# Kernel optimization log

Measured on AMD Instinct MI355X. Metric: run time of the kernel, lower is better.

## Reference

```python
import jax, jax.numpy as jnp
import numpy as np

DET = 512       # detector bins
N_THETA = 180   # projection angles, theta = 0..179 degrees (1 deg spacing)


def _ramp_filter(size):
    """skimage _get_fourier_filter(size, 'ramp'): spatial ramp -> FFT."""
    n = np.concatenate((np.arange(1, size // 2 + 1, 2),
                        np.arange(size // 2 - 1, 0, -2)))
    f = np.zeros(size)
    f[0] = 0.25
    f[1::2] = -1.0 / (np.pi * n) ** 2
    return jnp.asarray(2.0 * np.real(np.fft.fft(f)), dtype=jnp.float32)


def _iradon(x):
    B, C, det, A = x.shape
    theta = jnp.deg2rad(jnp.arange(A, dtype=jnp.float32))  # 0..179 deg

    # --- ramp filtering along the detector axis ---
    size = max(64, int(2 ** np.ceil(np.log2(2 * det))))  # 1024 for det=512
    filt = _ramp_filter(size)                            # (size,)
    xp = jnp.pad(x, ((0, 0), (0, 0), (0, size - det), (0, 0)))
    proj_f = jnp.fft.fft(xp, axis=2) * filt[None, None, :, None]
    filtered = jnp.real(jnp.fft.ifft(proj_f, axis=2))[:, :, :det, :]  # (B,C,det,A)

    # --- backprojection (circle=False) ---
    out_size = int(np.floor(np.sqrt(det ** 2 / 2.0)))  # 362
    radius = out_size // 2
    xpr = jnp.arange(out_size, dtype=jnp.float32)[:, None] - radius  # rows
    ypr = jnp.arange(out_size, dtype=jnp.float32)[None, :] - radius  # cols
    cos_t = jnp.cos(theta)
    sin_t = jnp.sin(theta)
    # detector coordinate for every (angle, pixel): t = y*cos - x*sin
    t = ypr[None] * cos_t[:, None, None] - xpr[None] * sin_t[:, None, None]  # (A,out,out)
    pos = t + det // 2          # index into detector axis (x = arange(det)-det//2)
    i0 = jnp.floor(pos).astype(jnp.int32)
    frac = pos - i0.astype(jnp.float32)
    in_range = ((pos >= 0) & (pos <= det - 1)).astype(jnp.float32)  # fill_value=0 outside
    i0c = jnp.clip(i0, 0, det - 1)
    i1c = jnp.clip(i0 + 1, 0, det - 1)

    P = out_size * out_size
    ft = jnp.moveaxis(filtered, 3, 2)                     # (B,C,A,det)
    idx0 = jnp.broadcast_to(i0c.reshape(A, P)[None, None], (B, C, A, P))
    idx1 = jnp.broadcast_to(i1c.reshape(A, P)[None, None], (B, C, A, P))
    g0 = jnp.take_along_axis(ft, idx0, axis=3)            # (B,C,A,P)
    g1 = jnp.take_along_axis(ft, idx1, axis=3)
    w = frac.reshape(A, P)[None, None]
    m = in_range.reshape(A, P)[None, None]
    val = ((1.0 - w) * g0 + w * g1) * m                   # bilinear-in-1D interp, 0 outside
    recon = val.sum(axis=2).reshape(B, C, out_size, out_size)
    return recon * (jnp.pi / (2.0 * A))


def setup_inputs() -> dict:
    key = jax.random.key(0)
    x = jax.random.normal(key, (4, 1, DET, N_THETA), dtype=jnp.float32)
    return {"x": x}


def reference(x):
    return _iradon(x)
```

## Files before the change

kernel.cpp:

```cpp
#include <hip/hip_runtime.h>
#include <math.h>

#define DET 512
#define NA  180
#define OUT 362
#define RAD 181
#define OUTSQ (OUT * OUT)
#define NB  4

#define NSPLIT 12
#define APB    15
#define CHUNK  3
#define LSTR   5
#define LLEN   (514 * LSTR)

constexpr double PI_D = 3.14159265358979323846;

constexpr double tsin(double x) {
    double x2 = x * x;
    return x * (1.0 + x2 * (-1.0/6 + x2 * (1.0/120 + x2 * (-1.0/5040 +
               x2 * (1.0/362880 + x2 * (-1.0/39916800))))));
}
constexpr double tcos(double x) {
    double x2 = x * x;
    return 1.0 + x2 * (-0.5 + x2 * (1.0/24 + x2 * (-1.0/720 +
               x2 * (1.0/40320 + x2 * (-1.0/3628800)))));
}

struct Trig { float c[NA]; float s[NA]; };
constexpr Trig make_trig() {
    Trig t{};
    constexpr double r = PI_D / 180.0;
    for (int k = 0; k < NA; ++k) {
        double c, s;
        if (k <= 45)       { c =  tcos(k * r);          s =  tsin(k * r); }
        else if (k <= 90)  { c =  tsin((90 - k) * r);   s =  tcos((90 - k) * r); }
        else if (k <= 135) { c = -tsin((k - 90) * r);   s =  tcos((k - 90) * r); }
        else               { c = -tcos((180 - k) * r);  s =  tsin((180 - k) * r); }
        t.c[k] = (float)c; t.s[k] = (float)s;
    }
    return t;
}
__device__ constexpr Trig TRIG = make_trig();

__host__ __device__ constexpr float rampw0(int m) {
    int a = m < 0 ? -m : m;
    if (a > 511 || (a & 1) == 0) return 0.0f;
    double md = (double)a;
    return (float)(-2.0 / (PI_D * PI_D * md * md));
}

template<int R>
__device__ __forceinline__ void tap(const float* __restrict__ p,
        float& a0, float& a1, float& a2, float& a3) {
    const float v = p[R];
    if constexpr (rampw0(R)      != 0.0f) a0 = fmaf(rampw0(R),      v, a0);
    if constexpr (rampw0(R - 32) != 0.0f) a1 = fmaf(rampw0(R - 32), v, a1);
    if constexpr (rampw0(R - 64) != 0.0f) a2 = fmaf(rampw0(R - 64), v, a2);
    if constexpr (rampw0(R - 96) != 0.0f) a3 = fmaf(rampw0(R - 96), v, a3);
}

template<int R, int REND>
__device__ __forceinline__ void sweep(const float* __restrict__ p,
        float& a0, float& a1, float& a2, float& a3) {
    if constexpr (R <= REND) {
        tap<R>(p, a0, a1, a2, a3);
        sweep<R + 2, REND>(p, a0, a1, a2, a3);
    }
}

__global__ __launch_bounds__(256) void ramp_filter_kernel(
        const float* __restrict__ x, float* __restrict__ ft) {
    const int a   = blockIdx.x;
    const int b   = blockIdx.y;
    const int tid = threadIdx.x;
    const int t    = tid & 127;
    const int half = tid >> 7;
    const int q = (t & 31) + 128 * (t >> 5);

    __shared__ float xs[3 * DET];
    __shared__ float red[4 * 128];

    xs[tid]        = 0.0f;
    xs[256 + tid]  = 0.0f;
    xs[1024 + tid] = 0.0f;
    xs[1280 + tid] = 0.0f;
    xs[512 + tid]  = x[(b * DET + tid) * NA + a];
    xs[768 + tid]  = x[(b * DET + 256 + tid) * NA + a];
    __syncthreads();

    const float* p = xs + 512 + q;
    float a0 = 0.0f, a1 = 0.0f, a2 = 0.0f, a3 = 0.0f;

    if (half == 0) {
        a0 = 0.5f * p[0];
        a1 = 0.5f * p[32];
        a2 = 0.5f * p[64];
        a3 = 0.5f * p[96];
        sweep<-511, 47>(p, a0, a1, a2, a3);
    } else {
        sweep<49, 607>(p, a0, a1, a2, a3);
        red[      t] = a0;
        red[128 + t] = a1;
        red[256 + t] = a2;
        red[384 + t] = a3;
    }
    __syncthreads();

    if (half == 0) {
        float* ob = ft + ((size_t)a * DET + q) * NB + b;
        ob[0]           = a0 + red[      t];
        ob[32 * NB]     = a1 + red[128 + t];
        ob[64 * NB]     = a2 + red[256 + t];
        ob[96 * NB]     = a3 + red[384 + t];
    }
}

__device__ __forceinline__ void acc4(float4& acc,
        const float* __restrict__ L, float pos) {
    float pf = floorf(pos);
    float fr = pos - pf;
    int   i0 = (int)pf;
    int   di = (pos > (float)(DET - 1)) ? (DET * LSTR) : (i0 * LSTR);
    const float* qp = L + di;
    float g0x = qp[0],        g0y = qp[1],        g0z = qp[2],        g0w = qp[3];
    float g1x = qp[LSTR + 0], g1y = qp[LSTR + 1], g1z = qp[LSTR + 2], g1w = qp[LSTR + 3];
    acc.x += fmaf(fr, g1x - g0x, g0x);
    acc.y += fmaf(fr, g1y - g0y, g0y);
    acc.z += fmaf(fr, g1z - g0z, g0z);
    acc.w += fmaf(fr, g1w - g0w, g0w);
}

__global__ __launch_bounds__(256) void backproject_kernel(
        const float4* __restrict__ ftq, float* __restrict__ out) {
    const int sp = blockIdx.z;
    const int r0 = blockIdx.y * 32;
    const int c0 = blockIdx.x * 32;
    const int tid = threadIdx.x;
    const int tx = tid & 15;
    const int ty = tid >> 4;

    __shared__ float lines[CHUNK][LLEN];

    if (tid < CHUNK * 10)
        lines[tid / 10][512 * LSTR + (tid % 10)] = 0.0f;

    const float xpr = (float)(min(r0 + ty, OUT - 1) - RAD);
    const float ypr = (float)(min(c0 + tx, OUT - 1) - RAD);

    float4 A00 = {0,0,0,0}, A01 = {0,0,0,0}, A10 = {0,0,0,0}, A11 = {0,0,0,0};

    for (int rd = 0; rd < APB / CHUNK; ++rd) {
        __syncthreads();
        const float4* g = ftq + (size_t)(sp * APB + rd * CHUNK) * DET;
        #pragma unroll
        for (int k = 0; k < CHUNK * DET / 256; ++k) {
            int j = tid + k * 256;
            float4 v = g[j];
            float* w = &lines[j >> 9][(j & 511) * LSTR];
            w[0] = v.x; w[1] = v.y; w[2] = v.z; w[3] = v.w;
        }
        __syncthreads();

        const int abase = sp * APB + rd * CHUNK;
        #pragma unroll
        for (int i = 0; i < CHUNK; ++i) {
            const float cv = TRIG.c[abase + i];
            const float sv = TRIG.s[abase + i];
            float p00 = fmaf(ypr, cv, fmaf(xpr, -sv, 256.0f));
            float p01 = fmaf(16.0f, cv, p00);
            float p10 = fmaf(-16.0f, sv, p00);
            float p11 = fmaf(-16.0f, sv, p01);
            const float* L = &lines[i][0];
            acc4(A00, L, p00);
            acc4(A01, L, p01);
            acc4(A10, L, p10);
            acc4(A11, L, p11);
        }
    }

    const float scale = (float)(PI_D / (2.0 * NA));
    const int r = r0 + ty;
    const int c = c0 + tx;

#define EMIT(ACC, RR, CC)                                          \
    if ((RR) < OUT && (CC) < OUT) {                                \
        const int off = (RR) * OUT + (CC);                         \
        atomicAdd(out + off,             (ACC).x * scale);         \
        atomicAdd(out + OUTSQ + off,     (ACC).y * scale);         \
        atomicAdd(out + 2 * OUTSQ + off, (ACC).z * scale);         \
        atomicAdd(out + 3 * OUTSQ + off, (ACC).w * scale);         \
    }
    EMIT(A00, r, c);
    EMIT(A01, r, c + 16);
    EMIT(A10, r + 16, c);
    EMIT(A11, r + 16, c + 16);
#undef EMIT
}

extern "C" void kernel_launch(void* const* d_in, const int* in_sizes, int n_in,
                              void* d_out, int out_size, void* d_ws, size_t ws_size,
                              hipStream_t stream) {
    const float* x = (const float*)d_in[0];
    float* ft  = (float*)d_ws;
    float* out = (float*)d_out;

    const int B = in_sizes[0] / (DET * NA);

    hipMemsetAsync(out, 0, (size_t)out_size * sizeof(float), stream);
    ramp_filter_kernel<<<dim3(NA, B), 256, 0, stream>>>(x, ft);
    backproject_kernel<<<dim3((OUT + 31) / 32, (OUT + 31) / 32, NSPLIT),
                         256, 0, stream>>>((const float4*)ft, out);
}
```

Baseline: 111.2 us.

## Gather backprojection samples directly from global memory instead of LDS staging

Removes the shared-memory staging of detector lines and the per-chunk barriers, so each thread now reads float4 samples straight from global memory and relies on the L1/L2 caches. Out-of-range handling becomes an index clamp plus a multiplicative mask instead of a padded zero entry. The angle split also changes from 12 to 15 splits of 12 angles, which adds blocks and atomics. The gathers now pay global or cache latency rather than LDS latency, and fewer angles per block means more atomic traffic.

Result: slower. 125.8 us (+13.2%).

```diff
diff --git a/kernel.cpp b/kernel.cpp
--- a/kernel.cpp
+++ b/kernel.cpp
@@ -8,11 +8,8 @@
 #define OUTSQ (OUT * OUT)
 #define NB  4
 
-#define NSPLIT 12
-#define APB    15
-#define CHUNK  3
-#define LSTR   5
-#define LLEN   (514 * LSTR)
+#define NSPLIT 15
+#define APB    12
 
 constexpr double PI_D = 3.14159265358979323846;
 
@@ -116,19 +113,18 @@
     }
 }
 
-__device__ __forceinline__ void acc4(float4& acc,
-        const float* __restrict__ L, float pos) {
-    float pf = floorf(pos);
-    float fr = pos - pf;
-    int   i0 = (int)pf;
-    int   di = (pos > (float)(DET - 1)) ? (DET * LSTR) : (i0 * LSTR);
-    const float* qp = L + di;
-    float g0x = qp[0],        g0y = qp[1],        g0z = qp[2],        g0w = qp[3];
-    float g1x = qp[LSTR + 0], g1y = qp[LSTR + 1], g1z = qp[LSTR + 2], g1w = qp[LSTR + 3];
-    acc.x += fmaf(fr, g1x - g0x, g0x);
-    acc.y += fmaf(fr, g1y - g0y, g0y);
-    acc.z += fmaf(fr, g1z - g0z, g0z);
-    acc.w += fmaf(fr, g1w - g0w, g0w);
+__device__ __forceinline__ void acc4g(float4& acc,
+        const float4* __restrict__ L, float pos) {
+    int   i0 = (int)pos;
+    i0 = min(i0, DET - 2);
+    float fr = pos - (float)i0;
+    float msk = pos <= (float)(DET - 1) ? 1.0f : 0.0f;
+    float4 g0 = L[i0];
+    float4 g1 = L[i0 + 1];
+    acc.x = fmaf(msk, fmaf(fr, g1.x - g0.x, g0.x), acc.x);
+    acc.y = fmaf(msk, fmaf(fr, g1.y - g0.y, g0.y), acc.y);
+    acc.z = fmaf(msk, fmaf(fr, g1.z - g0.z, g0.z), acc.z);
+    acc.w = fmaf(msk, fmaf(fr, g1.w - g0.w, g0.w), acc.w);
 }
 
 __global__ __launch_bounds__(256) void backproject_kernel(
@@ -140,43 +136,25 @@
     const int tx = tid & 15;
     const int ty = tid >> 4;
 
-    __shared__ float lines[CHUNK][LLEN];
-
-    if (tid < CHUNK * 10)
-        lines[tid / 10][512 * LSTR + (tid % 10)] = 0.0f;
-
     const float xpr = (float)(min(r0 + ty, OUT - 1) - RAD);
     const float ypr = (float)(min(c0 + tx, OUT - 1) - RAD);
 
     float4 A00 = {0,0,0,0}, A01 = {0,0,0,0}, A10 = {0,0,0,0}, A11 = {0,0,0,0};
 
-    for (int rd = 0; rd < APB / CHUNK; ++rd) {
-        __syncthreads();
-        const float4* g = ftq + (size_t)(sp * APB + rd * CHUNK) * DET;
-        #pragma unroll
-        for (int k = 0; k < CHUNK * DET / 256; ++k) {
-            int j = tid + k * 256;
-            float4 v = g[j];
-            float* w = &lines[j >> 9][(j & 511) * LSTR];
-            w[0] = v.x; w[1] = v.y; w[2] = v.z; w[3] = v.w;
-        }
-        __syncthreads();
-
-        const int abase = sp * APB + rd * CHUNK;
-        #pragma unroll
-        for (int i = 0; i < CHUNK; ++i) {
-            const float cv = TRIG.c[abase + i];
-            const float sv = TRIG.s[abase + i];
-            float p00 = fmaf(ypr, cv, fmaf(xpr, -sv, 256.0f));
-            float p01 = fmaf(16.0f, cv, p00);
-            float p10 = fmaf(-16.0f, sv, p00);
-            float p11 = fmaf(-16.0f, sv, p01);
-            const float* L = &lines[i][0];
-            acc4(A00, L, p00);
-            acc4(A01, L, p01);
-            acc4(A10, L, p10);
-            acc4(A11, L, p11);
-        }
+    const int ab = sp * APB;
+    #pragma unroll 2
+    for (int i = 0; i < APB; ++i) {
+        const float cv = TRIG.c[ab + i];
+        const float sv = TRIG.s[ab + i];
+        const float4* L = ftq + (size_t)(ab + i) * DET;
+        float p00 = fmaf(ypr, cv, fmaf(xpr, -sv, 256.0f));
+        float p01 = fmaf(16.0f, cv, p00);
+        float p10 = fmaf(-16.0f, sv, p00);
+        float p11 = fmaf(-16.0f, sv, p01);
+        acc4g(A00, L, p00);
+        acc4g(A01, L, p01);
+        acc4g(A10, L, p10);
+        acc4g(A11, L, p11);
     }
 
     const float scale = (float)(PI_D / (2.0 * NA));
```
